# Kernel tuning notes

Hardware: AMD Instinct MI355X
Metric: run time of the kernel (lower is better)

## Reference

```python
import jax, jax.numpy as jnp
import numpy as np

D_MODEL = 1024
NUM_HEADS = 16
D_HEAD = D_MODEL // NUM_HEADS
THETA = 10000.0


def _rope_tables(seq_len, d_k, theta):
    # inv_powers_k = theta**(-(2k-2)/d_k) for k=1..d_k/2 == theta**(-arange(0,d_k,2)/d_k)
    inv_powers = theta ** (-jnp.arange(0, d_k, 2, dtype=jnp.float32) / d_k)  # [d_k/2]
    positions = jnp.arange(seq_len, dtype=jnp.float32)
    angles = jnp.outer(positions, inv_powers)  # [S, d_k/2]
    return jnp.cos(angles), jnp.sin(angles)


def _apply_rope(x, cos, sin):
    # x: [..., S, d_k]; cos/sin: [S, d_k/2] broadcast over leading dims
    x_even = x[..., 0::2]
    x_odd = x[..., 1::2]
    r_even = x_even * cos - x_odd * sin
    r_odd = x_even * sin + x_odd * cos
    # interleave back: [..., S, d_k/2, 2] -> [..., S, d_k]
    return jnp.stack([r_even, r_odd], axis=-1).reshape(x.shape)


def setup_inputs() -> dict:
    key = jax.random.key(0)
    ks = jax.random.split(key, 5)
    B, S = 2, 2048
    sigma = (2.0 / (D_MODEL + D_MODEL)) ** 0.5
    x = jax.random.normal(ks[0], (B, S, D_MODEL), dtype=jnp.float32)
    wq = jax.random.normal(ks[1], (D_MODEL, D_MODEL), dtype=jnp.float32) * sigma
    wk = jax.random.normal(ks[2], (D_MODEL, D_MODEL), dtype=jnp.float32) * sigma
    wv = jax.random.normal(ks[3], (D_MODEL, D_MODEL), dtype=jnp.float32) * sigma
    wo = jax.random.normal(ks[4], (D_MODEL, D_MODEL), dtype=jnp.float32) * sigma
    return {"x": x, "wq": wq, "wk": wk, "wv": wv, "wo": wo}


def reference(x, wq, wk, wv, wo):
    B, S, D = x.shape
    H, Dh = NUM_HEADS, D_HEAD
    # Linear: einx.dot('... in, out in -> ... out') == x @ W.T
    q = jnp.einsum('bsd,od->bso', x, wq)
    k = jnp.einsum('bsd,od->bso', x, wk)
    v = jnp.einsum('bsd,od->bso', x, wv)
    # split heads: [B, S, H, Dh] -> [B, H, S, Dh]
    q = q.reshape(B, S, H, Dh).transpose(0, 2, 1, 3)
    k = k.reshape(B, S, H, Dh).transpose(0, 2, 1, 3)
    v = v.reshape(B, S, H, Dh).transpose(0, 2, 1, 3)
    cos, sin = _rope_tables(S, Dh, THETA)
    q = _apply_rope(q, cos, sin)
    k = _apply_rope(k, cos, sin)
    scale = 1.0 / jnp.sqrt(jnp.float32(Dh))
    scores = jnp.einsum('bhqd,bhkd->bhqk', q, k) * scale  # [B,H,S,S]
    causal = jnp.tril(jnp.ones((S, S), dtype=bool))
    scores = jnp.where(causal, scores, -jnp.inf)
    probs = jax.nn.softmax(scores, axis=-1)
    attn = jnp.einsum('bhqk,bhkd->bhqd', probs, v)
    attn = attn.transpose(0, 2, 1, 3).reshape(B, S, D)
    return jnp.einsum('bsd,od->bso', attn, wo)
```

## Files before the change

kernel.cpp:

```cpp
#include <hip/hip_runtime.h>
#include <hip/hip_bf16.h>
#include <math.h>

#define B_SZ   2
#define SEQ    2048
#define DM     1024
#define NH     16
#define DH     64
#define MROWS  (B_SZ * SEQ)
#define DQKV   (3 * DM)

typedef __attribute__((ext_vector_type(8))) short short8;
typedef __attribute__((ext_vector_type(4))) float f32x4;
typedef __attribute__((ext_vector_type(16))) float f32x16;
typedef __attribute__((ext_vector_type(4))) unsigned short us4;
typedef __attribute__((ext_vector_type(2))) unsigned int u32x2;

__device__ __forceinline__ float b2f(unsigned short u) {
    union { float f; unsigned int i; } x; x.i = ((unsigned int)u) << 16; return x.f;
}
__device__ __forceinline__ unsigned short f2b(float f) {
    union { float f; unsigned int i; } x; x.f = f;
    return (unsigned short)((x.i + 0x7fffu + ((x.i >> 16) & 1u)) >> 16);
}
__device__ __forceinline__ unsigned int pk2b(float a, float b) {
    float2 f2; f2.x = a; f2.y = b;
    __hip_bfloat162 hb = __float22bfloat162_rn(f2);
    return *reinterpret_cast<unsigned int*>(&hb);
}
__device__ __forceinline__ float fexp2(float x) {
    float r; asm("v_exp_f32 %0, %1" : "=v"(r) : "v"(x)); return r;
}
__device__ __forceinline__ void swap32(unsigned int& a, unsigned int& b) {
    asm("v_permlane32_swap_b32 %0, %1" : "+v"(a), "+v"(b));
}

__device__ __forceinline__ void gload_lds16(const unsigned short* g, unsigned short* lds_base_uniform) {
    __builtin_amdgcn_global_load_lds(
        (const __attribute__((address_space(1))) unsigned int*)g,
        (__attribute__((address_space(3))) unsigned int*)lds_base_uniform,
        16, 0, 0);
}

#define NX4 (MROWS * DM / 4)
#define NW4 (DM * DM / 4)

__global__ __launch_bounds__(256) void cvt_all(const float* __restrict__ x,
                                               const float* __restrict__ wq,
                                               const float* __restrict__ wk,
                                               const float* __restrict__ wv,
                                               const float* __restrict__ wo,
                                               unsigned short* __restrict__ xb,
                                               unsigned short* __restrict__ wqkv,
                                               unsigned short* __restrict__ wob,
                                               float* __restrict__ tab) {
    const int i = blockIdx.x * 256 + threadIdx.x;
    const int ncvt = NX4 + 4 * NW4;
    if (i < ncvt) {
        const float* src; unsigned short* dst; int off;
        if (i < NX4) { src = x; dst = xb; off = i; }
        else {
            int j = i - NX4;
            int w = j >> 18;
            off = j & (NW4 - 1);
            src = (w == 0) ? wq : (w == 1) ? wk : (w == 2) ? wv : wo;
            dst = (w < 3) ? wqkv + (size_t)w * DM * DM : wob;
        }
        float4 v = reinterpret_cast<const float4*>(src)[off];
        us4 o = { f2b(v.x), f2b(v.y), f2b(v.z), f2b(v.w) };
        reinterpret_cast<us4*>(dst)[off] = o;
    } else {
        int t = i - ncvt;
        if (t < SEQ * 32) {
            int s = t >> 5, fi = t & 31;
            float inv = powf(10000.0f, -(float)fi / 32.0f);
            float ang = (float)s * inv;
            tab[2 * t]     = cosf(ang);
            tab[2 * t + 1] = sinf(ang);
        }
    }
}

#define BM 128
#define BN 128
#define BK 32

__global__ __launch_bounds__(256, 2) void gemm_out(const unsigned short* __restrict__ A,
                                                   const unsigned short* __restrict__ B,
                                                   float* __restrict__ Cout) {
    __shared__ unsigned short As[3][128 * BK];
    __shared__ unsigned short Bs[3][64 * BK];
    const int tid  = threadIdx.x;
    const int lane = tid & 63, wid = tid >> 6;
    const int lm = lane & 15, lg = lane >> 4;
    const int brow = blockIdx.y * 128, bcol = blockIdx.x * 64;
    const int K = DM, N = DM;
    const int NT = K / BK;

    f32x4 acc[2][4] = {};

    const int rA  = tid >> 2;
    const int kc8 = (tid & 3) * 8;
    const unsigned short* gA0 = A + (size_t)(brow + rA) * K + kc8;
    const unsigned short* gA1 = A + (size_t)(brow + 64 + rA) * K + kc8;
    const unsigned short* gB0 = B + (size_t)(bcol + rA) * K + kc8;
    const int la = wid * 512;

#define OSTAGE(t, bi)                                        \
    {                                                        \
        const int _o = (t) * BK;                             \
        gload_lds16(gA0 + _o, &As[bi][la]);                  \
        gload_lds16(gA1 + _o, &As[bi][2048 + la]);           \
        gload_lds16(gB0 + _o, &Bs[bi][la]);                  \
    }

    OSTAGE(0, 0);
    OSTAGE(1, 1);
    asm volatile("s_waitcnt vmcnt(3)" ::: "memory");
    __builtin_amdgcn_s_barrier();
    asm volatile("" ::: "memory");

    int cb = 0, sb = 2;
    for (int k = 0; k < NT; ++k) {
        if (k + 2 < NT) OSTAGE(k + 2, sb);
        short8 a[2], b[4];
#pragma unroll
        for (int m = 0; m < 2; ++m)
            a[m] = *reinterpret_cast<const short8*>(&As[cb][(wid * 32 + m * 16 + lm) * BK + lg * 8]);
#pragma unroll
        for (int n = 0; n < 4; ++n)
            b[n] = *reinterpret_cast<const short8*>(&Bs[cb][(n * 16 + lm) * BK + lg * 8]);
#pragma unroll
        for (int m = 0; m < 2; ++m)
#pragma unroll
            for (int n = 0; n < 4; ++n)
                acc[m][n] = __builtin_amdgcn_mfma_f32_16x16x32_bf16(a[m], b[n], acc[m][n], 0, 0, 0);
        if (k + 1 < NT) {
            if (k + 2 < NT) asm volatile("s_waitcnt vmcnt(3)" ::: "memory");
            else            asm volatile("s_waitcnt vmcnt(0)" ::: "memory");
            __builtin_amdgcn_s_barrier();
            asm volatile("" ::: "memory");
        }
        cb = (cb == 2) ? 0 : cb + 1;
        sb = (sb == 2) ? 0 : sb + 1;
    }
#undef OSTAGE

#pragma unroll
    for (int m = 0; m < 2; ++m) {
#pragma unroll
        for (int r = 0; r < 4; ++r) {
            const size_t base = (size_t)(brow + wid * 32 + m * 16 + lg * 4 + r) * N + bcol + lm;
#pragma unroll
            for (int n = 0; n < 4; ++n)
                Cout[base + n * 16] = acc[m][n][r];
        }
    }
}

__global__ __launch_bounds__(256, 2) void gemm_qkv(const unsigned short* __restrict__ A,
                                                   const unsigned short* __restrict__ B,
                                                   unsigned short* __restrict__ qkv,
                                                   unsigned short* __restrict__ vT,
                                                   const float* __restrict__ tab) {
    __shared__ unsigned short As[3][BM * BK];
    __shared__ unsigned short Bs[3][BN * BK];
    const int tid  = threadIdx.x;
    const int lane = tid & 63, wid = tid >> 6;
    const int wr = wid >> 1, wc = wid & 1;
    const int lm = lane & 15, lg = lane >> 4;
    const int brow = blockIdx.y * BM, bcol = blockIdx.x * BN;
    const int K = DM;
    const int NT = K / BK;

    f32x4 acc[4][4] = {};

    const int rA  = tid >> 2;
    const int kc8 = (tid & 3) * 8;
    const unsigned short* gA0 = A + (size_t)(brow + rA) * K + kc8;
    const unsigned short* gA1 = A + (size_t)(brow + 64 + rA) * K + kc8;
    const unsigned short* gB0 = B + (size_t)(bcol + rA) * K + kc8;
    const unsigned short* gB1 = B + (size_t)(bcol + 64 + rA) * K + kc8;
    const int la = wid * 512;

#define QSTAGE(t, bi)                                        \
    {                                                        \
        const int _o = (t) * BK;                             \
        gload_lds16(gA0 + _o, &As[bi][la]);                  \
        gload_lds16(gA1 + _o, &As[bi][2048 + la]);           \
        gload_lds16(gB0 + _o, &Bs[bi][la]);                  \
        gload_lds16(gB1 + _o, &Bs[bi][2048 + la]);           \
    }

    QSTAGE(0, 0);
    QSTAGE(1, 1);
    asm volatile("s_waitcnt vmcnt(4)" ::: "memory");
    __builtin_amdgcn_s_barrier();
    asm volatile("" ::: "memory");

    int cb = 0, sb = 2;
    for (int k = 0; k < NT; ++k) {
        if (k + 2 < NT) QSTAGE(k + 2, sb);
        short8 a[4], b[4];
#pragma unroll
        for (int m = 0; m < 4; ++m)
            a[m] = *reinterpret_cast<const short8*>(&As[cb][(wr * 64 + m * 16 + lm) * BK + lg * 8]);
#pragma unroll
        for (int n = 0; n < 4; ++n)
            b[n] = *reinterpret_cast<const short8*>(&Bs[cb][(wc * 64 + n * 16 + lm) * BK + lg * 8]);
#pragma unroll
        for (int m = 0; m < 4; ++m)
#pragma unroll
            for (int n = 0; n < 4; ++n)
                acc[m][n] = __builtin_amdgcn_mfma_f32_16x16x32_bf16(a[m], b[n], acc[m][n], 0, 0, 0);
        if (k + 1 < NT) {
            if (k + 2 < NT) asm volatile("s_waitcnt vmcnt(4)" ::: "memory");
            else            asm volatile("s_waitcnt vmcnt(0)" ::: "memory");
            __builtin_amdgcn_s_barrier();
            asm volatile("" ::: "memory");
        }
        cb = (cb == 2) ? 0 : cb + 1;
        sb = (sb == 2) ? 0 : sb + 1;
    }
#undef QSTAGE

    const int reg = blockIdx.x >> 3;
    if (reg < 2) {
        const float qs = (reg == 0) ? (0.125f * 1.4426950408889634f) : 1.0f;
        const int odd = lm & 1;
#pragma unroll
        for (int m = 0; m < 4; ++m) {
#pragma unroll
            for (int r = 0; r < 4; ++r) {
                const int row = brow + wr * 64 + m * 16 + lg * 4 + r;
                const int s   = row & (SEQ - 1);
                const size_t base = (size_t)row * DQKV + bcol + wc * 64 + lm;
#pragma unroll
                for (int n = 0; n < 4; ++n) {
                    float v  = acc[m][n][r];
                    float pv = __shfl_xor(v, 1);
                    const int fi = (n * 16 + lm) >> 1;
                    float2 cs = reinterpret_cast<const float2*>(tab)[s * 32 + fi];
                    float c = cs.x * qs, sn = cs.y * qs;
                    float out = odd ? (pv * sn + v * c) : (v * c - pv * sn);
                    qkv[base + n * 16] = f2b(out);
                }
            }
        }
    } else {
        const int b = brow >> 11;
#pragma unroll
        for (int m = 0; m < 4; ++m) {
            const int s0 = (brow + wr * 64 + m * 16 + lg * 4) & (SEQ - 1);
#pragma unroll
            for (int n = 0; n < 4; ++n) {
                const int vcol = bcol + wc * 64 + n * 16 + lm - 2 * DM;
                const int h = vcol >> 6, d = vcol & 63;
                us4 val = { f2b(acc[m][n][0]), f2b(acc[m][n][1]),
                            f2b(acc[m][n][2]), f2b(acc[m][n][3]) };
                *reinterpret_cast<us4*>(vT + (size_t)((b * NH + h) * DH + d) * SEQ + s0) = val;
            }
        }
    }
}

__global__ __launch_bounds__(256, 2) void attn_mfma(const unsigned short* __restrict__ qkv,
                                                    const unsigned short* __restrict__ vT,
                                                    unsigned short* __restrict__ o) {
    const int tid  = threadIdx.x;
    const int wid  = tid >> 6;
    const int lane = tid & 63;
    const int l31 = lane & 31, lo = lane >> 5;

    const int bid = blockIdx.x;
    const int u   = bid >> 3;
    const int j   = u & 31, hi = u >> 5;
    const int bh_hi = (hi ? 2 : 0) + (j >> 4);
    const int chunk = hi ? (15 - (j & 15)) : (j & 15);
    const int bh = (bid & 7) + 8 * bh_hi;
    const int b = bh >> 4, h = bh & 15;
    const int qbase = chunk * 128 + wid * 32;
    const int nb = 2 * chunk + 2;

    __shared__ unsigned short Kl[2][4096];
    __shared__ unsigned short Vl[2][4096];

    const unsigned short* kb = qkv + ((size_t)b * SEQ) * DQKV + DM + h * DH;
    const unsigned short* vb = vT + ((size_t)bh) * DH * SEQ;

    const int pr  = tid >> 4;
    const int st  = tid & 15;
    const int c16 = st ^ pr;
    const int hf  = c16 >> 3;
    const int cc  = c16 & 7;
    const unsigned short* kst0 = kb + (size_t)(pr + hf * 32) * DQKV + cc * 8;
    const unsigned short* kst1 = kst0 + (size_t)16 * DQKV;
    const unsigned short* vst0 = vb + (size_t)(pr + hf * 32) * SEQ + cc * 8;
    const unsigned short* vst1 = vst0 + 16 * SEQ;
    const int sdst = wid * 512;

    const unsigned short* qr = qkv + ((size_t)(b * SEQ + qbase + l31)) * DQKV + h * DH + lo * 8;
    short8 qb4[4];
#pragma unroll
    for (int dc = 0; dc < 4; ++dc)
        qb4[dc] = *reinterpret_cast<const short8*>(qr + dc * 16);

    f32x16 oA = {0,0,0,0,0,0,0,0,0,0,0,0,0,0,0,0};
    f32x16 oB = {0,0,0,0,0,0,0,0,0,0,0,0,0,0,0,0};
    float mrun = -INFINITY, lrun = 0.f;

    gload_lds16(kst0, &Kl[0][sdst]);
    gload_lds16(kst1, &Kl[0][2048 + sdst]);
    gload_lds16(vst0, &Vl[0][sdst]);
    gload_lds16(vst1, &Vl[0][2048 + sdst]);
    __syncthreads();

    const int lx = l31 & 15;
    int buf = 0;
    for (int blk = 0; blk < nb; ++blk) {
        const int kbase = blk << 6;

        if (blk + 1 < nb) {
            const size_t ko = (size_t)(kbase + 64) * DQKV;
            const int    vo = kbase + 64;
            gload_lds16(kst0 + ko, &Kl[buf ^ 1][sdst]);
            gload_lds16(kst1 + ko, &Kl[buf ^ 1][2048 + sdst]);
            gload_lds16(vst0 + vo, &Vl[buf ^ 1][sdst]);
            gload_lds16(vst1 + vo, &Vl[buf ^ 1][2048 + sdst]);
        }

        const char* Kb = (const char*)&Kl[buf][0];
        const char* Vb = (const char*)&Vl[buf][0];

        f32x16 S0 = {0,0,0,0,0,0,0,0,0,0,0,0,0,0,0,0};
        f32x16 S1 = {0,0,0,0,0,0,0,0,0,0,0,0,0,0,0,0};
        __builtin_amdgcn_s_setprio(1);
#pragma unroll
        for (int dc = 0; dc < 4; ++dc) {
            const int s0s = ((dc * 2 + lo)     ^ lx) << 4;
            const int s1s = ((8 + dc * 2 + lo) ^ lx) << 4;
            short8 k0 = *reinterpret_cast<const short8*>(Kb + l31 * 256 + s0s);
            short8 k1 = *reinterpret_cast<const short8*>(Kb + l31 * 256 + s1s);
            S0 = __builtin_amdgcn_mfma_f32_32x32x16_bf16(k0, qb4[dc], S0, 0, 0, 0);
            S1 = __builtin_amdgcn_mfma_f32_32x32x16_bf16(k1, qb4[dc], S1, 0, 0, 0);
        }
        __builtin_amdgcn_s_setprio(0);

        short8 vf[4][2];
#pragma unroll
        for (int kc = 0; kc < 4; ++kc) {
#pragma unroll
            for (int dh = 0; dh < 2; ++dh) {
                const int sts = ((dh * 8 + kc * 2 + lo) ^ lx) << 4;
                vf[kc][dh] = *reinterpret_cast<const short8*>(Vb + l31 * 256 + sts);
            }
        }

        float s0[16], s1[16];
#pragma unroll
        for (int r = 0; r < 16; ++r) { s0[r] = S0[r]; s1[r] = S1[r]; }

        if (blk + 2 >= nb) {
            const int q = qbase + l31;
#pragma unroll
            for (int r = 0; r < 16; ++r) {
                const int kk = kbase + (r & 3) + 8 * (r >> 2) + 4 * lo;
                s0[r] = (kk <= q) ? s0[r] : -INFINITY;
                s1[r] = (kk + 32 <= q) ? s1[r] : -INFINITY;
            }
        }

        float tmax[8];
#pragma unroll
        for (int i = 0; i < 8; ++i)
            tmax[i] = fmaxf(fmaxf(s0[2 * i], s0[2 * i + 1]), fmaxf(s1[2 * i], s1[2 * i + 1]));
        float lmax = fmaxf(fmaxf(fmaxf(tmax[0], tmax[1]), fmaxf(tmax[2], tmax[3])),
                           fmaxf(fmaxf(tmax[4], tmax[5]), fmaxf(tmax[6], tmax[7])));

        if (!__all(lmax - mrun <= 8.0f)) {
            float mx = fmaxf(lmax, __shfl_xor(lmax, 32));
            float mn = fmaxf(mrun, mx);
            float fsc = fexp2(mrun - mn);
            mrun = mn;
            lrun *= fsc;
#pragma unroll
            for (int r = 0; r < 16; ++r) {
                float fr = __shfl(fsc, (r & 3) + 8 * (r >> 2) + 4 * lo);
                oA[r] *= fr; oB[r] *= fr;
            }
        }

#pragma unroll
        for (int r = 0; r < 16; ++r) { s0[r] = fexp2(s0[r] - mrun); s1[r] = fexp2(s1[r] - mrun); }

        float ac[8];
#pragma unroll
        for (int i = 0; i < 8; ++i)
            ac[i] = (s0[2 * i] + s0[2 * i + 1]) + (s1[2 * i] + s1[2 * i + 1]);
        float ps = ((ac[0] + ac[1]) + (ac[2] + ac[3])) + ((ac[4] + ac[5]) + (ac[6] + ac[7]));
        ps += __shfl_xor(ps, 32);
        lrun += ps;

        unsigned int pf[4][4];
#pragma unroll
        for (int s = 0; s < 2; ++s) {
            const float* sp = s ? s1 : s0;
            unsigned int a0 = pk2b(sp[0], sp[1]);
            unsigned int b0 = pk2b(sp[4], sp[5]);
            swap32(a0, b0);
            unsigned int a1 = pk2b(sp[2], sp[3]);
            unsigned int b1 = pk2b(sp[6], sp[7]);
            swap32(a1, b1);
            pf[2 * s][0] = a0; pf[2 * s][1] = a1; pf[2 * s][2] = b0; pf[2 * s][3] = b1;
            unsigned int a2 = pk2b(sp[8], sp[9]);
            unsigned int b2 = pk2b(sp[12], sp[13]);
            swap32(a2, b2);
            unsigned int a3 = pk2b(sp[10], sp[11]);
            unsigned int b3 = pk2b(sp[14], sp[15]);
            swap32(a3, b3);
            pf[2 * s + 1][0] = a2; pf[2 * s + 1][1] = a3; pf[2 * s + 1][2] = b2; pf[2 * s + 1][3] = b3;
        }

        __builtin_amdgcn_s_setprio(1);
#pragma unroll
        for (int kc = 0; kc < 4; ++kc) {
            union { unsigned int u[4]; short8 v; } P;
            P.u[0] = pf[kc][0]; P.u[1] = pf[kc][1]; P.u[2] = pf[kc][2]; P.u[3] = pf[kc][3];
            oA = __builtin_amdgcn_mfma_f32_32x32x16_bf16(P.v, vf[kc][0], oA, 0, 0, 0);
            oB = __builtin_amdgcn_mfma_f32_32x32x16_bf16(P.v, vf[kc][1], oB, 0, 0, 0);
        }
        __builtin_amdgcn_s_setprio(0);

        __syncthreads();
        buf ^= 1;
    }

    const float rl = 1.0f / lrun;
#pragma unroll
    for (int r = 0; r < 16; ++r) {
        const int qr2 = (r & 3) + 8 * (r >> 2) + 4 * lo;
        const float linv = __shfl(rl, qr2);
        const size_t rowoff = ((size_t)(b * SEQ + qbase + qr2)) * DM + h * DH;
        o[rowoff + l31]      = f2b(oA[r] * linv);
        o[rowoff + 32 + l31] = f2b(oB[r] * linv);
    }
}

extern "C" void kernel_launch(void* const* d_in, const int* in_sizes, int n_in,
                              void* d_out, int out_size, void* d_ws, size_t ws_size,
                              hipStream_t stream) {
    const float* x  = (const float*)d_in[0];
    const float* wq = (const float*)d_in[1];
    const float* wk = (const float*)d_in[2];
    const float* wv = (const float*)d_in[3];
    const float* wo = (const float*)d_in[4];
    float* out = (float*)d_out;

    char* ws = (char*)d_ws;
    const size_t MB = 1024 * 1024;
    unsigned short* xb      = (unsigned short*)(ws);
    unsigned short* wqkv    = (unsigned short*)(ws + 8 * MB);
    unsigned short* wob     = (unsigned short*)(ws + 14 * MB);
    unsigned short* qkv     = (unsigned short*)(ws + 16 * MB);
    unsigned short* vT      = (unsigned short*)(ws + 40 * MB);
    float*          ropetab = (float*)(ws + 48 * MB);
    unsigned short* attn_bf = xb;

    const int cvt_grid = (NX4 + 4 * NW4 + SEQ * 32) / 256;
    cvt_all<<<cvt_grid, 256, 0, stream>>>(x, wq, wk, wv, wo, xb, wqkv, wob, ropetab);

    gemm_qkv<<<dim3(DQKV / BN, MROWS / BM), 256, 0, stream>>>(xb, wqkv, qkv, vT, ropetab);

    attn_mfma<<<512, 256, 0, stream>>>(qkv, vT, attn_bf);

    gemm_out<<<dim3(DM / 64, MROWS / 128), 256, 0, stream>>>(attn_bf, wob, out);
}
```

Baseline: 117.5 us.

## Split attention KV blocks across wave pairs and double block count

Each attention block now covers 64 query rows instead of 128. Within a block, two waves share each 32-row query tile and each handles half of every 64-key block, then merge their partial softmax states (max, sum, output) through LDS at the end. The grid doubles to 1024 blocks and launch bounds target 4 blocks per CU, aiming for better occupancy and less causal load imbalance. The cost is extra LDS traffic, a merge step with many shuffles, and each K/V tile being loaded per 64 queries rather than per 128, which doubles K/V global traffic.

After: 112.8 us, median of 3. -4.0%, faster.

```diff
diff --git a/kernel.cpp b/kernel.cpp
--- a/kernel.cpp
+++ b/kernel.cpp
@@ -264,23 +264,25 @@
     }
 }
 
-__global__ __launch_bounds__(256, 2) void attn_mfma(const unsigned short* __restrict__ qkv,
+__global__ __launch_bounds__(256, 4) void attn_mfma(const unsigned short* __restrict__ qkv,
                                                     const unsigned short* __restrict__ vT,
                                                     unsigned short* __restrict__ o) {
     const int tid  = threadIdx.x;
     const int wid  = tid >> 6;
     const int lane = tid & 63;
     const int l31 = lane & 31, lo = lane >> 5;
+    const int tile = wid >> 1;
+    const int half = wid & 1;
 
     const int bid = blockIdx.x;
     const int u   = bid >> 3;
-    const int j   = u & 31, hi = u >> 5;
-    const int bh_hi = (hi ? 2 : 0) + (j >> 4);
-    const int chunk = hi ? (15 - (j & 15)) : (j & 15);
+    const int j   = u & 31;
+    const int bh_hi = u >> 5;
+    const int chunk = (bh_hi & 1) ? (31 - j) : j;
     const int bh = (bid & 7) + 8 * bh_hi;
     const int b = bh >> 4, h = bh & 15;
-    const int qbase = chunk * 128 + wid * 32;
-    const int nb = 2 * chunk + 2;
+    const int qbase = chunk * 64 + tile * 32;
+    const int nb = chunk + 1;
 
     __shared__ unsigned short Kl[2][4096];
     __shared__ unsigned short Vl[2][4096];
@@ -307,7 +309,7 @@
 
     f32x16 oA = {0,0,0,0,0,0,0,0,0,0,0,0,0,0,0,0};
     f32x16 oB = {0,0,0,0,0,0,0,0,0,0,0,0,0,0,0,0};
-    float mrun = -INFINITY, lrun = 0.f;
+    float mrun = -3.0e38f, lrun = 0.f;
 
     gload_lds16(kst0, &Kl[0][sdst]);
     gload_lds16(kst1, &Kl[0][2048 + sdst]);
@@ -332,50 +334,45 @@
         const char* Kb = (const char*)&Kl[buf][0];
         const char* Vb = (const char*)&Vl[buf][0];
 
-        f32x16 S0 = {0,0,0,0,0,0,0,0,0,0,0,0,0,0,0,0};
-        f32x16 S1 = {0,0,0,0,0,0,0,0,0,0,0,0,0,0,0,0};
+        f32x16 S = {0,0,0,0,0,0,0,0,0,0,0,0,0,0,0,0};
         __builtin_amdgcn_s_setprio(1);
 #pragma unroll
         for (int dc = 0; dc < 4; ++dc) {
-            const int s0s = ((dc * 2 + lo)     ^ lx) << 4;
-            const int s1s = ((8 + dc * 2 + lo) ^ lx) << 4;
-            short8 k0 = *reinterpret_cast<const short8*>(Kb + l31 * 256 + s0s);
-            short8 k1 = *reinterpret_cast<const short8*>(Kb + l31 * 256 + s1s);
-            S0 = __builtin_amdgcn_mfma_f32_32x32x16_bf16(k0, qb4[dc], S0, 0, 0, 0);
-            S1 = __builtin_amdgcn_mfma_f32_32x32x16_bf16(k1, qb4[dc], S1, 0, 0, 0);
+            const int ss = ((half * 8 + dc * 2 + lo) ^ lx) << 4;
+            short8 k0 = *reinterpret_cast<const short8*>(Kb + l31 * 256 + ss);
+            S = __builtin_amdgcn_mfma_f32_32x32x16_bf16(k0, qb4[dc], S, 0, 0, 0);
         }
         __builtin_amdgcn_s_setprio(0);
 
-        short8 vf[4][2];
-#pragma unroll
-        for (int kc = 0; kc < 4; ++kc) {
+        short8 vf[2][2];
+#pragma unroll
+        for (int kc = 0; kc < 2; ++kc) {
 #pragma unroll
             for (int dh = 0; dh < 2; ++dh) {
-                const int sts = ((dh * 8 + kc * 2 + lo) ^ lx) << 4;
+                const int sts = ((dh * 8 + (half * 2 + kc) * 2 + lo) ^ lx) << 4;
                 vf[kc][dh] = *reinterpret_cast<const short8*>(Vb + l31 * 256 + sts);
             }
         }
 
-        float s0[16], s1[16];
-#pragma unroll
-        for (int r = 0; r < 16; ++r) { s0[r] = S0[r]; s1[r] = S1[r]; }
-
-        if (blk + 2 >= nb) {
+        float s[16];
+#pragma unroll
+        for (int r = 0; r < 16; ++r) s[r] = S[r];
+
+        if (blk == nb - 1) {
             const int q = qbase + l31;
 #pragma unroll
             for (int r = 0; r < 16; ++r) {
-                const int kk = kbase + (r & 3) + 8 * (r >> 2) + 4 * lo;
-                s0[r] = (kk <= q) ? s0[r] : -INFINITY;
-                s1[r] = (kk + 32 <= q) ? s1[r] : -INFINITY;
+                const int kk = kbase + half * 32 + (r & 3) + 8 * (r >> 2) + 4 * lo;
+                s[r] = (kk <= q) ? s[r] : -INFINITY;
             }
         }
 
-        float tmax[8];
-#pragma unroll
-        for (int i = 0; i < 8; ++i)
-            tmax[i] = fmaxf(fmaxf(s0[2 * i], s0[2 * i + 1]), fmaxf(s1[2 * i], s1[2 * i + 1]));
-        float lmax = fmaxf(fmaxf(fmaxf(tmax[0], tmax[1]), fmaxf(tmax[2], tmax[3])),
-                           fmaxf(fmaxf(tmax[4], tmax[5]), fmaxf(tmax[6], tmax[7])));
+        float t0 = fmaxf(s[0], s[1]),  t1 = fmaxf(s[2], s[3]);
+        float t2 = fmaxf(s[4], s[5]),  t3 = fmaxf(s[6], s[7]);
+        float t4 = fmaxf(s[8], s[9]),  t5 = fmaxf(s[10], s[11]);
+        float t6 = fmaxf(s[12], s[13]), t7 = fmaxf(s[14], s[15]);
+        float lmax = fmaxf(fmaxf(fmaxf(t0, t1), fmaxf(t2, t3)),
+                           fmaxf(fmaxf(t4, t5), fmaxf(t6, t7)));
 
         if (!__all(lmax - mrun <= 8.0f)) {
             float mx = fmaxf(lmax, __shfl_xor(lmax, 32));
@@ -391,39 +388,37 @@
         }
 
 #pragma unroll
-        for (int r = 0; r < 16; ++r) { s0[r] = fexp2(s0[r] - mrun); s1[r] = fexp2(s1[r] - mrun); }
-
-        float ac[8];
-#pragma unroll
-        for (int i = 0; i < 8; ++i)
-            ac[i] = (s0[2 * i] + s0[2 * i + 1]) + (s1[2 * i] + s1[2 * i + 1]);
-        float ps = ((ac[0] + ac[1]) + (ac[2] + ac[3])) + ((ac[4] + ac[5]) + (ac[6] + ac[7]));
+        for (int r = 0; r < 16; ++r) s[r] = fexp2(s[r] - mrun);
+
+        float a0 = (s[0] + s[1]) + (s[2] + s[3]);
+        float a1 = (s[4] + s[5]) + (s[6] + s[7]);
+        float a2 = (s[8] + s[9]) + (s[10] + s[11]);
+        float a3 = (s[12] + s[13]) + (s[14] + s[15]);
+        float ps = (a0 + a1) + (a2 + a3);
         ps += __shfl_xor(ps, 32);
         lrun += ps;
 
-        unsigned int pf[4][4];
-#pragma unroll
-        for (int s = 0; s < 2; ++s) {
-            const float* sp = s ? s1 : s0;
-            unsigned int a0 = pk2b(sp[0], sp[1]);
-            unsigned int b0 = pk2b(sp[4], sp[5]);
-            swap32(a0, b0);
-            unsigned int a1 = pk2b(sp[2], sp[3]);
-            unsigned int b1 = pk2b(sp[6], sp[7]);
-            swap32(a1, b1);
-            pf[2 * s][0] = a0; pf[2 * s][1] = a1; pf[2 * s][2] = b0; pf[2 * s][3] = b1;
-            unsigned int a2 = pk2b(sp[8], sp[9]);
-            unsigned int b2 = pk2b(sp[12], sp[13]);
-            swap32(a2, b2);
-            unsigned int a3 = pk2b(sp[10], sp[11]);
-            unsigned int b3 = pk2b(sp[14], sp[15]);
-            swap32(a3, b3);
-            pf[2 * s + 1][0] = a2; pf[2 * s + 1][1] = a3; pf[2 * s + 1][2] = b2; pf[2 * s + 1][3] = b3;
+        unsigned int pf[2][4];
+        {
+            unsigned int a0u = pk2b(s[0], s[1]);
+            unsigned int b0u = pk2b(s[4], s[5]);
+            swap32(a0u, b0u);
+            unsigned int a1u = pk2b(s[2], s[3]);
+            unsigned int b1u = pk2b(s[6], s[7]);
+            swap32(a1u, b1u);
+            pf[0][0] = a0u; pf[0][1] = a1u; pf[0][2] = b0u; pf[0][3] = b1u;
+            unsigned int a2u = pk2b(s[8], s[9]);
+            unsigned int b2u = pk2b(s[12], s[13]);
+            swap32(a2u, b2u);
+            unsigned int a3u = pk2b(s[10], s[11]);
+            unsigned int b3u = pk2b(s[14], s[15]);
+            swap32(a3u, b3u);
+            pf[1][0] = a2u; pf[1][1] = a3u; pf[1][2] = b2u; pf[1][3] = b3u;
         }
 
         __builtin_amdgcn_s_setprio(1);
 #pragma unroll
-        for (int kc = 0; kc < 4; ++kc) {
+        for (int kc = 0; kc < 2; ++kc) {
             union { unsigned int u[4]; short8 v; } P;
             P.u[0] = pf[kc][0]; P.u[1] = pf[kc][1]; P.u[2] = pf[kc][2]; P.u[3] = pf[kc][3];
             oA = __builtin_amdgcn_mfma_f32_32x32x16_bf16(P.v, vf[kc][0], oA, 0, 0, 0);
@@ -435,14 +430,45 @@
         buf ^= 1;
     }
 
-    const float rl = 1.0f / lrun;
-#pragma unroll
-    for (int r = 0; r < 16; ++r) {
-        const int qr2 = (r & 3) + 8 * (r >> 2) + 4 * lo;
-        const float linv = __shfl(rl, qr2);
-        const size_t rowoff = ((size_t)(b * SEQ + qbase + qr2)) * DM + h * DH;
-        o[rowoff + l31]      = f2b(oA[r] * linv);
-        o[rowoff + 32 + l31] = f2b(oB[r] * linv);
+    float* mbase = (tile == 0) ? (float*)&Kl[0][0] : (float*)&Vl[0][0];
+    if (half == 0) {
+#pragma unroll
+        for (int g = 0; g < 8; ++g) {
+            f32x4 w;
+#pragma unroll
+            for (int t = 0; t < 4; ++t)
+                w[t] = (g < 4) ? oA[(g & 3) * 4 + t] : oB[(g & 3) * 4 + t];
+            *reinterpret_cast<f32x4*>(mbase + lane * 32 + ((g ^ (lane & 7)) * 4)) = w;
+        }
+        if (lo == 0) {
+            mbase[2048 + l31 * 2]     = mrun;
+            mbase[2048 + l31 * 2 + 1] = lrun;
+        }
+    }
+    __syncthreads();
+    if (half == 1) {
+        const float m0 = mbase[2048 + l31 * 2];
+        const float l0 = mbase[2048 + l31 * 2 + 1];
+        const float ms = fmaxf(m0, mrun);
+        const float f0 = fexp2(m0 - ms);
+        const float f1 = fexp2(mrun - ms);
+        const float li = 1.0f / (l0 * f0 + lrun * f1);
+#pragma unroll
+        for (int g = 0; g < 8; ++g) {
+            f32x4 rd = *reinterpret_cast<const f32x4*>(mbase + lane * 32 + ((g ^ (lane & 7)) * 4));
+#pragma unroll
+            for (int t = 0; t < 4; ++t) {
+                const int r = (g & 3) * 4 + t;
+                const float mine = (g < 4) ? oA[r] : oB[r];
+                const int qr2 = (r & 3) + 8 * (r >> 2) + 4 * lo;
+                const float f0q = __shfl(f0, qr2);
+                const float f1q = __shfl(f1, qr2);
+                const float liq = __shfl(li, qr2);
+                const float val = (rd[t] * f0q + mine * f1q) * liq;
+                const size_t rowoff = ((size_t)(b * SEQ + qbase + qr2)) * DM + h * DH + ((g < 4) ? 0 : 32);
+                o[rowoff + l31] = f2b(val);
+            }
+        }
     }
 }
 
@@ -471,7 +497,7 @@
 
     gemm_qkv<<<dim3(DQKV / BN, MROWS / BM), 256, 0, stream>>>(xb, wqkv, qkv, vT, ropetab);
 
-    attn_mfma<<<512, 256, 0, stream>>>(qkv, vT, attn_bf);
+    attn_mfma<<<1024, 256, 0, stream>>>(qkv, vT, attn_bf);
 
     gemm_out<<<dim3(DM / 64, MROWS / 128), 256, 0, stream>>>(attn_bf, wob, out);
 }
```
